# Kernel tuning notes

Measured on AMD Instinct MI355X. Metric: run time of the kernel, lower is better.

## Reference

```python
import jax, jax.numpy as jnp
import numpy as np

N = 10000       # nodes
E = 160000      # edges (avg degree 16)
F_IN = 5        # node feature dim
ED = 2          # edge feature dim


def _tconv(x, src, dst, ea, Wq, bq, Wk, bk, Wv, bv, We, Ws, bs, heads, C, concat):
    """PyG TransformerConv (eval mode, root_weight=True, beta=False)."""
    n = x.shape[0]
    q = (x @ Wq + bq).reshape(n, heads, C)
    k = (x @ Wk + bk).reshape(n, heads, C)
    v = (x @ Wv + bv).reshape(n, heads, C)
    e = (ea @ We).reshape(ea.shape[0], heads, C)          # edge embedding, added to key and value
    kj = k[src] + e                                        # [E,H,C] gather source keys
    vj = v[src] + e                                        # [E,H,C] gather source values
    logits = jnp.einsum('ehc,ehc->eh', q[dst], kj) / jnp.sqrt(jnp.asarray(C, x.dtype))
    m = jax.ops.segment_max(logits, dst, num_segments=n)   # stable segment softmax over in-edges
    p = jnp.exp(logits - m[dst])
    s = jax.ops.segment_sum(p, dst, num_segments=n)
    alpha = p / s[dst]                                     # [E,H]
    out = jax.ops.segment_sum(alpha[..., None] * vj, dst, num_segments=n)  # [N,H,C]
    out = out.reshape(n, heads * C) if concat else jnp.mean(out, axis=1)
    return out + x @ Ws + bs                               # root/skip connection


def setup_inputs() -> dict:
    key = jax.random.key(0)
    keys = iter(jax.random.split(key, 64))
    def p(shape):
        return jax.random.normal(next(keys), shape, jnp.float32) * 0.05
    inp = {}
    inp['x'] = jax.random.normal(next(keys), (N, F_IN), jnp.float32)
    inp['edge_src'] = jax.random.randint(next(keys), (E,), 0, N)
    inp['edge_dst'] = jax.random.randint(next(keys), (E,), 0, N)
    inp['edge_attr'] = jax.random.normal(next(keys), (E, ED), jnp.float32)
    # (in_dim, heads, out_channels, concat) for the 3 TransformerConv layers
    layers = [(F_IN, 4, 128, True), (512, 4, 128, True), (512, 1, 64, False)]
    for i, (fin, h, c, concat) in enumerate(layers, 1):
        hc = h * c
        sk = hc if concat else c
        inp[f'Wq{i}'] = p((fin, hc)); inp[f'bq{i}'] = p((hc,))
        inp[f'Wk{i}'] = p((fin, hc)); inp[f'bk{i}'] = p((hc,))
        inp[f'Wv{i}'] = p((fin, hc)); inp[f'bv{i}'] = p((hc,))
        inp[f'We{i}'] = p((ED, hc))   # lin_edge has no bias in PyG
        inp[f'Ws{i}'] = p((fin, sk)); inp[f'bs{i}'] = p((sk,))
    return inp


def reference(x, edge_src, edge_dst, edge_attr,
              Wq1, bq1, Wk1, bk1, Wv1, bv1, We1, Ws1, bs1,
              Wq2, bq2, Wk2, bk2, Wv2, bv2, We2, Ws2, bs2,
              Wq3, bq3, Wk3, bk3, Wv3, bv3, We3, Ws3, bs3):
    h = jax.nn.relu(_tconv(x, edge_src, edge_dst, edge_attr,
                           Wq1, bq1, Wk1, bk1, Wv1, bv1, We1, Ws1, bs1, 4, 128, True))
    h = jax.nn.relu(_tconv(h, edge_src, edge_dst, edge_attr,
                           Wq2, bq2, Wk2, bk2, Wv2, bv2, We2, Ws2, bs2, 4, 128, True))
    return _tconv(h, edge_src, edge_dst, edge_attr,
                  Wq3, bq3, Wk3, bk3, Wv3, bv3, We3, Ws3, bs3, 1, 64, False)
```

## Files before the change

kernel.cpp:

```cpp
#include <hip/hip_runtime.h>

typedef unsigned short u16;
typedef __attribute__((ext_vector_type(8))) short bf16x8;
typedef __attribute__((ext_vector_type(4))) float f32x4;

__device__ __forceinline__ float bf2f(u16 s) {
    return __uint_as_float(((unsigned)s) << 16);
}
__device__ __forceinline__ u16 f2bf(float f) {
    unsigned u = __float_as_uint(f);
    u += 0x7fff + ((u >> 16) & 1);
    return (u16)(u >> 16);
}
__device__ __forceinline__ void unpack8(bf16x8 x, float* f) {
#pragma unroll
    for (int j = 0; j < 8; ++j) f[j] = bf2f((u16)x[j]);
}

struct Ptr8 { const float* p[8]; };
struct PrepArgs { const float* w[8]; const float* b[8]; };

__global__ __launch_bounds__(256)
void prep_weights(PrepArgs a, u16* __restrict__ Wt2, u16* __restrict__ Wt3,
                  float* __restrict__ b2, float* __restrict__ b3) {
    int z = blockIdx.z;
    if (z == 8) {
        if (blockIdx.y != 0 || blockIdx.x >= 9) return;
        int j = blockIdx.x * 256 + threadIdx.x;
        if (j < 2048) b2[j] = a.b[j >> 9][j & 511];
        else if (j < 2304) { int jj = j - 2048; b3[jj] = a.b[4 + (jj >> 6)][jj & 63]; }
        return;
    }
    const float* in;
    u16* out;
    int Nw;
    if (z < 4) { in = a.w[z]; out = Wt2 + (size_t)z * 512 * 512; Nw = 512; }
    else {
        if (blockIdx.y >= 2) return;
        in = a.w[z]; out = Wt3 + (size_t)(z - 4) * 64 * 512; Nw = 64;
    }
    __shared__ float t[32][33];
    int kb = blockIdx.x * 32, nb = blockIdx.y * 32;
    int tx = threadIdx.x & 31, ty = threadIdx.x >> 5;
#pragma unroll
    for (int r = ty; r < 32; r += 8)
        if (nb + tx < Nw)
            t[r][tx] = in[(size_t)(kb + r) * Nw + nb + tx];
    __syncthreads();
#pragma unroll
    for (int r = ty; r < 32; r += 8)
        if (nb + r < Nw)
            out[(size_t)(nb + r) * 512 + kb + tx] = f2bf(t[tx][r]);
}

__global__ __launch_bounds__(256)
void gemm_l1(const float* __restrict__ X, Ptr8 wb, u16* __restrict__ OUT, int N) {
    int wsel = threadIdx.x >> 6;
    int jj = (threadIdx.x & 63) * 8;
    const float* W = wb.p[wsel];
    const float* b = wb.p[4 + wsel];
    float w[5][8], bs[8];
#pragma unroll
    for (int i = 0; i < 5; ++i)
#pragma unroll
        for (int j = 0; j < 8; ++j) w[i][j] = W[(size_t)i * 512 + jj + j];
#pragma unroll
    for (int j = 0; j < 8; ++j) bs[j] = b[jj + j];
    int n0 = blockIdx.x * 8;
    int nend = (N - n0 < 8) ? (N - n0) : 8;
    for (int i = 0; i < nend; ++i) {
        int n = n0 + i;
        float xr[5];
#pragma unroll
        for (int k = 0; k < 5; ++k) xr[k] = X[(size_t)n * 5 + k];
        float acc[8];
#pragma unroll
        for (int j = 0; j < 8; ++j) acc[j] = bs[j];
#pragma unroll
        for (int k = 0; k < 5; ++k)
#pragma unroll
            for (int j = 0; j < 8; ++j) acc[j] = fmaf(xr[k], w[k][j], acc[j]);
        bf16x8 o;
#pragma unroll
        for (int j = 0; j < 8; ++j) o[j] = (short)f2bf(acc[j]);
        *(bf16x8*)(OUT + (size_t)n * 2048 + wsel * 512 + jj) = o;
    }
}

template <int TN>
__global__ __launch_bounds__(256)
void gemm_bf16(const u16* __restrict__ A, const u16* __restrict__ Bt,
               const float* __restrict__ bias, u16* __restrict__ C,
               int M, int Ncols, int K) {
    constexpr int TM = 128, BK = 64;
    constexpr int MFR = (TN == 128) ? 4 : 2;
    constexpr int NFR = 4;
    constexpr int ACH = TM * BK / (256 * 8);
    constexpr int BCH = TN * BK / (256 * 8);

    __shared__ u16 As[TM * BK];
    __shared__ u16 Bs[TN * BK];

    int tid = threadIdx.x;
    int lane = tid & 63;
    int w = tid >> 6;
    int rowbase = blockIdx.x * TM;
    int colbase = blockIdx.y * TN;
    int mwave = (TN == 128) ? (w >> 1) * 64 : w * 32;
    int nwave = (TN == 128) ? (w & 1) * 64 : 0;

    f32x4 acc[MFR][NFR] = {};

    for (int k0 = 0; k0 < K; k0 += BK) {
        bf16x8 ra[ACH], rb[BCH];
#pragma unroll
        for (int c = 0; c < ACH; ++c) {
            int idx = c * 256 + tid;
            int row = idx >> 3, sl = idx & 7;
            int gr = rowbase + row; if (gr > M - 1) gr = M - 1;
            ra[c] = *(const bf16x8*)(A + (size_t)gr * K + k0 + sl * 8);
        }
#pragma unroll
        for (int c = 0; c < BCH; ++c) {
            int idx = c * 256 + tid;
            int row = idx >> 3, sl = idx & 7;
            rb[c] = *(const bf16x8*)(Bt + (size_t)(colbase + row) * K + k0 + sl * 8);
        }
        __syncthreads();
#pragma unroll
        for (int c = 0; c < ACH; ++c) {
            int idx = c * 256 + tid;
            int row = idx >> 3, sl = idx & 7;
            *(bf16x8*)&As[row * BK + ((sl ^ (row & 7)) * 8)] = ra[c];
        }
#pragma unroll
        for (int c = 0; c < BCH; ++c) {
            int idx = c * 256 + tid;
            int row = idx >> 3, sl = idx & 7;
            *(bf16x8*)&Bs[row * BK + ((sl ^ (row & 7)) * 8)] = rb[c];
        }
        __syncthreads();
#pragma unroll
        for (int kh = 0; kh < 2; ++kh) {
            bf16x8 af[MFR], bfr[NFR];
            int ks = (lane >> 4) + kh * 4;
#pragma unroll
            for (int mi = 0; mi < MFR; ++mi) {
                int r = mwave + mi * 16 + (lane & 15);
                af[mi] = *(const bf16x8*)&As[r * BK + ((ks ^ (r & 7)) * 8)];
            }
#pragma unroll
            for (int ni = 0; ni < NFR; ++ni) {
                int r = nwave + ni * 16 + (lane & 15);
                bfr[ni] = *(const bf16x8*)&Bs[r * BK + ((ks ^ (r & 7)) * 8)];
            }
#pragma unroll
            for (int mi = 0; mi < MFR; ++mi)
#pragma unroll
                for (int ni = 0; ni < NFR; ++ni)
                    acc[mi][ni] = __builtin_amdgcn_mfma_f32_16x16x32_bf16(
                        af[mi], bfr[ni], acc[mi][ni], 0, 0, 0);
        }
    }
#pragma unroll
    for (int mi = 0; mi < MFR; ++mi) {
        int r0 = rowbase + mwave + mi * 16 + (lane >> 4) * 4;
#pragma unroll
        for (int ni = 0; ni < NFR; ++ni) {
            int col = colbase + nwave + ni * 16 + (lane & 15);
            float bv = bias[col];
#pragma unroll
            for (int r = 0; r < 4; ++r) {
                int row = r0 + r;
                if (row < M)
                    C[(size_t)row * Ncols + col] = f2bf(acc[mi][ni][r] + bv);
            }
        }
    }
}

__global__ __launch_bounds__(256)
void histo_dst(const int* __restrict__ dst, int* __restrict__ deg, int E) {
    int i = blockIdx.x * 256 + threadIdx.x;
    if (i < E) atomicAdd(&deg[dst[i]], 1);
}

__global__ __launch_bounds__(1024)
void scan_deg(const int* __restrict__ deg, int* __restrict__ off,
              int* __restrict__ cur, int N) {
    __shared__ int part[1024];
    int t = threadIdx.x;
    int per = (N + 1023) / 1024;
    int base = t * per;
    int s = 0;
    for (int i = 0; i < per; ++i)
        if (base + i < N) s += deg[base + i];
    part[t] = s;
    __syncthreads();
    for (int d = 1; d < 1024; d <<= 1) {
        int v = (t >= d) ? part[t - d] : 0;
        __syncthreads();
        part[t] += v;
        __syncthreads();
    }
    int excl = (t > 0) ? part[t - 1] : 0;
    for (int i = 0; i < per; ++i) {
        int n = base + i;
        if (n < N) {
            off[n] = excl;
            cur[n] = excl;
            excl += deg[n];
        }
    }
    if (t == 1023) off[N] = part[1023];
}

__global__ __launch_bounds__(256)
void scatter_edges(const int* __restrict__ src, const int* __restrict__ dst,
                   const float* __restrict__ EA, int* __restrict__ cur,
                   int* __restrict__ csrc, float2* __restrict__ caxy, int E) {
    int i = blockIdx.x * 256 + threadIdx.x;
    if (i < E) {
        int p = atomicAdd(&cur[dst[i]], 1);
        csrc[p] = src[i];
        caxy[p] = *(const float2*)(EA + 2 * (size_t)i);
    }
}

template <int H, int C, int LPG, int EPAR, bool RELU, typename OutT>
__global__ __launch_bounds__(256)
void node_attn(const u16* __restrict__ QKVS, int SR, int koff, int voff,
               int skoff, const int* __restrict__ csrc,
               const float2* __restrict__ caxy, const float* __restrict__ We,
               const int* __restrict__ off, OutT* __restrict__ OUT,
               int OST, int N, float scale) {
    constexpr int HC = H * C;
    constexpr int NG = 64 / LPG;
    int n = blockIdx.x * 4 + (threadIdx.x >> 6);
    if (n >= N) return;
    int lane = threadIdx.x & 63;
    int g = lane / LPG;
    int li = lane % LPG;
    int cc = (EPAR > 1 ? 0 : g) * C + li * 8;

    const u16* nrow = QKVS + (size_t)n * SR;
    float q[8];
    unpack8(*(const bf16x8*)(nrow + cc), q);

    float qw0 = 0.f, qw1 = 0.f;
    {
        f32x4 wa = *(const f32x4*)(We + cc), wb = *(const f32x4*)(We + cc + 4);
        f32x4 wc = *(const f32x4*)(We + HC + cc), wd = *(const f32x4*)(We + HC + cc + 4);
#pragma unroll
        for (int j = 0; j < 4; ++j) {
            qw0 = fmaf(q[j], wa[j], qw0); qw0 = fmaf(q[4 + j], wb[j], qw0);
            qw1 = fmaf(q[j], wc[j], qw1); qw1 = fmaf(q[4 + j], wd[j], qw1);
        }
    }
#pragma unroll
    for (int d = 1; d < LPG; d <<= 1) {
        qw0 += __shfl_xor(qw0, d);
        qw1 += __shfl_xor(qw1, d);
    }

    int base = off[n];
    int deg = off[n + 1] - base;
    int pdeg = deg < 64 ? deg : 64;
    int ps = 0; float pax = 0.f, pay = 0.f;
    if (lane < pdeg) {
        ps = csrc[base + lane];
        float2 a = caxy[base + lane];
        pax = a.x; pay = a.y;
    }

    float m = -1e30f, s = 0.f, A0 = 0.f, A1 = 0.f;
    float acc[8] = {};
    const u16* Kp = QKVS + koff;
    const u16* Vp = QKVS + voff;

    auto process = [&](float ax, float ay, bf16x8 k8, bf16x8 v8) {
        float kf[8];
        unpack8(k8, kf);
        float qk = 0.f;
#pragma unroll
        for (int j = 0; j < 8; ++j) qk = fmaf(q[j], kf[j], qk);
#pragma unroll
        for (int d = 1; d < LPG; d <<= 1) qk += __shfl_xor(qk, d);
        float lg = scale * (qk + ax * qw0 + ay * qw1);
        if (lg > m + 8.f) {
            float r = __expf(m - lg);
            s *= r; A0 *= r; A1 *= r;
#pragma unroll
            for (int j = 0; j < 8; ++j) acc[j] *= r;
            m = lg;
        }
        float p = __expf(lg - m);
        s += p;
        A0 = fmaf(p, ax, A0);
        A1 = fmaf(p, ay, A1);
        float vf[8];
        unpack8(v8, vf);
#pragma unroll
        for (int j = 0; j < 8; ++j) acc[j] = fmaf(p, vf[j], acc[j]);
    };

    if constexpr (EPAR == 1) {
        auto ldp = [&](int t, bf16x8& k8, bf16x8& v8) {
            int tt = t < pdeg ? t : 0;
            int s0 = __shfl(ps, tt);
            k8 = *(const bf16x8*)(Kp + (size_t)s0 * SR + cc);
            v8 = *(const bf16x8*)(Vp + (size_t)s0 * SR + cc);
        };
        if (pdeg > 0) {
            bf16x8 ka0, va0, ka1, va1, kb0, vb0, kb1, vb1;
            ldp(0, ka0, va0); ldp(1, ka1, va1);
            ldp(2, kb0, vb0); ldp(3, kb1, vb1);
            int t = 0;
            for (; t + 2 < pdeg; t += 4) {
                float ax, ay;
                ax = __shfl(pax, t); ay = __shfl(pay, t);
                process(ax, ay, ka0, va0);
                ax = __shfl(pax, t + 1); ay = __shfl(pay, t + 1);
                process(ax, ay, ka1, va1);
                ldp(t + 4, ka0, va0); ldp(t + 5, ka1, va1);
                ax = __shfl(pax, t + 2); ay = __shfl(pay, t + 2);
                process(ax, ay, kb0, vb0);
                if (t + 3 < pdeg) {
                    ax = __shfl(pax, t + 3); ay = __shfl(pay, t + 3);
                    process(ax, ay, kb1, vb1);
                }
                ldp(t + 6, kb0, vb0); ldp(t + 7, kb1, vb1);
            }
            if (t < pdeg) {
                float ax = __shfl(pax, t), ay = __shfl(pay, t);
                process(ax, ay, ka0, va0);
            }
            if (t + 1 < pdeg) {
                float ax = __shfl(pax, t + 1), ay = __shfl(pay, t + 1);
                process(ax, ay, ka1, va1);
            }
        }
        for (int t = 64; t < deg; ++t) {
            int s0 = csrc[base + t];
            float2 a = caxy[base + t];
            bf16x8 k0 = *(const bf16x8*)(Kp + (size_t)s0 * SR + cc);
            bf16x8 v0 = *(const bf16x8*)(Vp + (size_t)s0 * SR + cc);
            process(a.x, a.y, k0, v0);
        }
    } else {
        int trips = (pdeg + NG - 1) / NG;
        for (int k = 0; k < trips; ++k) {
            int idx = g + NG * k;
            bool valid = idx < pdeg;
            int sidx = valid ? idx : (pdeg - 1);
            int s0 = __shfl(ps, sidx);
            float ax0 = __shfl(pax, sidx), ay0 = __shfl(pay, sidx);
            bf16x8 k0 = *(const bf16x8*)(Kp + (size_t)s0 * SR + cc);
            bf16x8 v0 = *(const bf16x8*)(Vp + (size_t)s0 * SR + cc);
            if (valid) process(ax0, ay0, k0, v0);
        }
        int otr = (deg > 64) ? (deg - 64 + NG - 1) / NG : 0;
        for (int k = 0; k < otr; ++k) {
            int idx = 64 + NG * k + g;
            bool valid = idx < deg;
            int ii = valid ? idx : (deg - 1);
            int s0 = csrc[base + ii];
            float2 a = caxy[base + ii];
            bf16x8 k0 = *(const bf16x8*)(Kp + (size_t)s0 * SR + cc);
            bf16x8 v0 = *(const bf16x8*)(Vp + (size_t)s0 * SR + cc);
            if (valid) process(a.x, a.y, k0, v0);
        }
#pragma unroll
        for (int d = LPG; d < 64; d <<= 1) {
            float mo = __shfl_xor(m, d), so = __shfl_xor(s, d);
            float A0o = __shfl_xor(A0, d), A1o = __shfl_xor(A1, d);
            float mn = fmaxf(m, mo);
            float ra = __expf(m - mn), rb = __expf(mo - mn);
            s = s * ra + so * rb;
            A0 = A0 * ra + A0o * rb;
            A1 = A1 * ra + A1o * rb;
#pragma unroll
            for (int j = 0; j < 8; ++j) {
                float ao = __shfl_xor(acc[j], d);
                acc[j] = acc[j] * ra + ao * rb;
            }
            m = mn;
        }
    }

    if (EPAR == 1 || g == 0) {
        float inv = (s > 0.f) ? 1.f / s : 0.f;
        float sk[8];
        unpack8(*(const bf16x8*)(nrow + skoff + cc), sk);
        f32x4 wa = *(const f32x4*)(We + cc), wb = *(const f32x4*)(We + cc + 4);
        f32x4 wc = *(const f32x4*)(We + HC + cc), wd = *(const f32x4*)(We + HC + cc + 4);
        float w0[8] = {wa[0], wa[1], wa[2], wa[3], wb[0], wb[1], wb[2], wb[3]};
        float w1[8] = {wc[0], wc[1], wc[2], wc[3], wd[0], wd[1], wd[2], wd[3]};
        float o[8];
#pragma unroll
        for (int j = 0; j < 8; ++j) {
            float agg = (acc[j] + A0 * w0[j] + A1 * w1[j]) * inv;
            o[j] = agg + sk[j];
            if (RELU) o[j] = fmaxf(o[j], 0.f);
        }
        if constexpr (sizeof(OutT) == 2) {
            bf16x8 ov;
#pragma unroll
            for (int j = 0; j < 8; ++j) ov[j] = (short)f2bf(o[j]);
            *(bf16x8*)((u16*)OUT + (size_t)n * OST + cc) = ov;
        } else {
            f32x4 oa = {o[0], o[1], o[2], o[3]}, ob = {o[4], o[5], o[6], o[7]};
            *(f32x4*)((float*)OUT + (size_t)n * OST + cc) = oa;
            *(f32x4*)((float*)OUT + (size_t)n * OST + cc + 4) = ob;
        }
    }
}

extern "C" void kernel_launch(void* const* d_in, const int* in_sizes, int n_in,
                              void* d_out, int out_size, void* d_ws, size_t ws_size,
                              hipStream_t stream) {
    const float* x  = (const float*)d_in[0];
    const int* esrc = (const int*)d_in[1];
    const int* edst = (const int*)d_in[2];
    const float* ea = (const float*)d_in[3];
    const int N = in_sizes[0] / 5;
    const int E = in_sizes[1];
    auto in = [&](int i) { return (const float*)d_in[i]; };

    char* p = (char*)d_ws;
    auto alloc = [&](size_t b) {
        char* r = p; p += (b + 255) & ~(size_t)255; return (void*)r;
    };
    u16* QKVS  = (u16*)alloc((size_t)N * 2048 * 2);
    u16* HB    = (u16*)alloc((size_t)N * 512 * 2);
    u16* Wt2   = (u16*)alloc((size_t)2048 * 512 * 2);
    u16* Wt3   = (u16*)alloc((size_t)256 * 512 * 2);
    float* b2  = (float*)alloc(2048 * 4);
    float* b3  = (float*)alloc(256 * 4);
    int* deg   = (int*)alloc((size_t)N * 4);
    int* off   = (int*)alloc((size_t)(N + 1) * 4);
    int* cur   = (int*)alloc((size_t)N * 4);
    int* csrc  = (int*)alloc((size_t)E * 4);
    float2* caxy = (float2*)alloc((size_t)E * 8);

    dim3 b256(256);
    int gE256 = (E + 255) / 256;
    int gM = (N + 127) / 128;
    int gA = (N + 3) / 4;
    const float scale128 = 0.08838834764831845f;
    const float scale64  = 0.125f;

    hipMemsetAsync(deg, 0, (size_t)N * sizeof(int), stream);
    histo_dst<<<gE256, b256, 0, stream>>>(edst, deg, E);
    scan_deg<<<1, 1024, 0, stream>>>(deg, off, cur, N);
    scatter_edges<<<gE256, b256, 0, stream>>>(esrc, edst, ea, cur, csrc, caxy, E);

    PrepArgs pa = {{in(13), in(15), in(17), in(20), in(22), in(24), in(26), in(29)},
                   {in(14), in(16), in(18), in(21), in(23), in(25), in(27), in(30)}};
    prep_weights<<<dim3(16, 16, 9), b256, 0, stream>>>(pa, Wt2, Wt3, b2, b3);

    Ptr8 l1 = {{in(4), in(6), in(8), in(11), in(5), in(7), in(9), in(12)}};
    gemm_l1<<<dim3((N + 7) / 8), b256, 0, stream>>>(x, l1, QKVS, N);
    node_attn<4, 128, 16, 1, true, u16><<<dim3(gA), b256, 0, stream>>>(
        QKVS, 2048, 512, 1024, 1536, csrc, caxy, in(10), off, HB, 512, N, scale128);

    gemm_bf16<128><<<dim3(gM, 16), b256, 0, stream>>>(HB, Wt2, b2, QKVS, N, 2048, 512);
    node_attn<4, 128, 16, 1, true, u16><<<dim3(gA), b256, 0, stream>>>(
        QKVS, 2048, 512, 1024, 1536, csrc, caxy, in(19), off, HB, 512, N, scale128);

    gemm_bf16<64><<<dim3(gM, 4), b256, 0, stream>>>(HB, Wt3, b3, QKVS, N, 256, 512);
    node_attn<1, 64, 8, 8, false, float><<<dim3(gA), b256, 0, stream>>>(
        QKVS, 256, 64, 128, 192, csrc, caxy, in(28), off,
        (float*)d_out, 64, N, scale64);
}
```

Before: 225.8 us.

## Split node edges across four waves per block for 4-head attention layers

Adds a node_attn4 kernel that gives each node a whole 256-thread block. The four waves each take every fourth in-edge, and the partial online-softmax states are merged through shared memory. The goal is to cut the serial per-node edge loop and raise memory-level parallelism for the gather-heavy layers 1 and 2. The cost is a __syncthreads, shared-memory traffic and a merge step, plus three of four waves sitting idle during the final write. The old generic kernel is reduced to the layer-3 path only.

```diff
diff --git a/kernel.cpp b/kernel.cpp
--- a/kernel.cpp
+++ b/kernel.cpp
@@ -227,6 +227,169 @@
     }
 }
 
+template <bool RELU>
+__global__ __launch_bounds__(256)
+void node_attn4(const u16* __restrict__ QKVS, const int* __restrict__ csrc,
+                const float2* __restrict__ caxy, const float* __restrict__ We,
+                const int* __restrict__ off, u16* __restrict__ OUT,
+                int N, float scale) {
+    constexpr int SR = 2048, koff = 512, voff = 1024, skoff = 1536;
+    constexpr int HC = 512, C = 128, LPG = 16;
+    int n = blockIdx.x;
+    int w = threadIdx.x >> 6;
+    int lane = threadIdx.x & 63;
+    int g = lane / LPG;
+    int li = lane % LPG;
+    int cc = g * C + li * 8;
+
+    const u16* nrow = QKVS + (size_t)n * SR;
+    float q[8];
+    unpack8(*(const bf16x8*)(nrow + cc), q);
+
+    float qw0 = 0.f, qw1 = 0.f;
+    {
+        f32x4 wa = *(const f32x4*)(We + cc), wb = *(const f32x4*)(We + cc + 4);
+        f32x4 wc = *(const f32x4*)(We + HC + cc), wd = *(const f32x4*)(We + HC + cc + 4);
+#pragma unroll
+        for (int j = 0; j < 4; ++j) {
+            qw0 = fmaf(q[j], wa[j], qw0); qw0 = fmaf(q[4 + j], wb[j], qw0);
+            qw1 = fmaf(q[j], wc[j], qw1); qw1 = fmaf(q[4 + j], wd[j], qw1);
+        }
+    }
+#pragma unroll
+    for (int d = 1; d < LPG; d <<= 1) {
+        qw0 += __shfl_xor(qw0, d);
+        qw1 += __shfl_xor(qw1, d);
+    }
+
+    int base = off[n];
+    int deg = off[n + 1] - base;
+    int pdeg = deg < 64 ? deg : 64;
+    int ps = 0; float pax = 0.f, pay = 0.f;
+    int el = w + 4 * lane;
+    if (lane < 16 && el < pdeg) {
+        ps = csrc[base + el];
+        float2 a = caxy[base + el];
+        pax = a.x; pay = a.y;
+    }
+    int wdeg = (pdeg > w) ? ((pdeg - w + 3) >> 2) : 0;
+
+    float m = -1e30f, s = 0.f, A0 = 0.f, A1 = 0.f;
+    float acc[8] = {};
+    const u16* Kp = QKVS + koff;
+    const u16* Vp = QKVS + voff;
+
+    auto process = [&](float ax, float ay, bf16x8 k8, bf16x8 v8) {
+        float kf[8];
+        unpack8(k8, kf);
+        float qk = 0.f;
+#pragma unroll
+        for (int j = 0; j < 8; ++j) qk = fmaf(q[j], kf[j], qk);
+#pragma unroll
+        for (int d = 1; d < LPG; d <<= 1) qk += __shfl_xor(qk, d);
+        float lg = scale * (qk + ax * qw0 + ay * qw1);
+        if (lg > m + 8.f) {
+            float r = __expf(m - lg);
+            s *= r; A0 *= r; A1 *= r;
+#pragma unroll
+            for (int j = 0; j < 8; ++j) acc[j] *= r;
+            m = lg;
+        }
+        float p = __expf(lg - m);
+        s += p;
+        A0 = fmaf(p, ax, A0);
+        A1 = fmaf(p, ay, A1);
+        float vf[8];
+        unpack8(v8, vf);
+#pragma unroll
+        for (int j = 0; j < 8; ++j) acc[j] = fmaf(p, vf[j], acc[j]);
+    };
+
+    auto ldp = [&](int t, bf16x8& k8, bf16x8& v8) {
+        int tt = t < wdeg ? t : 0;
+        int s0 = __shfl(ps, tt);
+        k8 = *(const bf16x8*)(Kp + (size_t)s0 * SR + cc);
+        v8 = *(const bf16x8*)(Vp + (size_t)s0 * SR + cc);
+    };
+    if (wdeg > 0) {
+        bf16x8 ka0, va0, ka1, va1, kb0, vb0, kb1, vb1;
+        ldp(0, ka0, va0); ldp(1, ka1, va1);
+        ldp(2, kb0, vb0); ldp(3, kb1, vb1);
+        int t = 0;
+        for (; t + 2 < wdeg; t += 4) {
+            float ax, ay;
+            ax = __shfl(pax, t); ay = __shfl(pay, t);
+            process(ax, ay, ka0, va0);
+            ax = __shfl(pax, t + 1); ay = __shfl(pay, t + 1);
+            process(ax, ay, ka1, va1);
+            ldp(t + 4, ka0, va0); ldp(t + 5, ka1, va1);
+            ax = __shfl(pax, t + 2); ay = __shfl(pay, t + 2);
+            process(ax, ay, kb0, vb0);
+            if (t + 3 < wdeg) {
+                ax = __shfl(pax, t + 3); ay = __shfl(pay, t + 3);
+                process(ax, ay, kb1, vb1);
+            }
+            ldp(t + 6, kb0, vb0); ldp(t + 7, kb1, vb1);
+        }
+        if (t < wdeg) {
+            float ax = __shfl(pax, t), ay = __shfl(pay, t);
+            process(ax, ay, ka0, va0);
+        }
+        if (t + 1 < wdeg) {
+            float ax = __shfl(pax, t + 1), ay = __shfl(pay, t + 1);
+            process(ax, ay, ka1, va1);
+        }
+    }
+    for (int idx = 64 + w; idx < deg; idx += 4) {
+        int s0 = csrc[base + idx];
+        float2 a = caxy[base + idx];
+        bf16x8 k0 = *(const bf16x8*)(Kp + (size_t)s0 * SR + cc);
+        bf16x8 v0 = *(const bf16x8*)(Vp + (size_t)s0 * SR + cc);
+        process(a.x, a.y, k0, v0);
+    }
+
+    __shared__ float sm[3][64][13];
+    if (w > 0) {
+        float* d = sm[w - 1][lane];
+        d[0] = m; d[1] = s; d[2] = A0; d[3] = A1;
+#pragma unroll
+        for (int j = 0; j < 8; ++j) d[4 + j] = acc[j];
+    }
+    __syncthreads();
+    if (w == 0) {
+#pragma unroll
+        for (int wv = 0; wv < 3; ++wv) {
+            const float* d = sm[wv][lane];
+            float mo = d[0], so = d[1], A0o = d[2], A1o = d[3];
+            float mn = fmaxf(m, mo);
+            float ra = __expf(m - mn), rb = __expf(mo - mn);
+            s = s * ra + so * rb;
+            A0 = A0 * ra + A0o * rb;
+            A1 = A1 * ra + A1o * rb;
+#pragma unroll
+            for (int j = 0; j < 8; ++j)
+                acc[j] = acc[j] * ra + d[4 + j] * rb;
+            m = mn;
+        }
+        float inv = (s > 0.f) ? 1.f / s : 0.f;
+        float sk[8];
+        unpack8(*(const bf16x8*)(nrow + skoff + cc), sk);
+        f32x4 wa = *(const f32x4*)(We + cc), wb = *(const f32x4*)(We + cc + 4);
+        f32x4 wc = *(const f32x4*)(We + HC + cc), wd = *(const f32x4*)(We + HC + cc + 4);
+        float w0[8] = {wa[0], wa[1], wa[2], wa[3], wb[0], wb[1], wb[2], wb[3]};
+        float w1[8] = {wc[0], wc[1], wc[2], wc[3], wd[0], wd[1], wd[2], wd[3]};
+        bf16x8 ov;
+#pragma unroll
+        for (int j = 0; j < 8; ++j) {
+            float agg = (acc[j] + A0 * w0[j] + A1 * w1[j]) * inv;
+            float o = agg + sk[j];
+            if (RELU) o = fmaxf(o, 0.f);
+            ov[j] = (short)f2bf(o);
+        }
+        *(bf16x8*)(OUT + (size_t)n * 512 + cc) = ov;
+    }
+}
+
 template <int H, int C, int LPG, int EPAR, bool RELU, typename OutT>
 __global__ __launch_bounds__(256)
 void node_attn(const u16* __restrict__ QKVS, int SR, int koff, int voff,
@@ -241,7 +404,7 @@
     int lane = threadIdx.x & 63;
     int g = lane / LPG;
     int li = lane % LPG;
-    int cc = (EPAR > 1 ? 0 : g) * C + li * 8;
+    int cc = li * 8;
 
     const u16* nrow = QKVS + (size_t)n * SR;
     float q[8];
@@ -304,91 +467,46 @@
         for (int j = 0; j < 8; ++j) acc[j] = fmaf(p, vf[j], acc[j]);
     };
 
-    if constexpr (EPAR == 1) {
-        auto ldp = [&](int t, bf16x8& k8, bf16x8& v8) {
-            int tt = t < pdeg ? t : 0;
-            int s0 = __shfl(ps, tt);
-            k8 = *(const bf16x8*)(Kp + (size_t)s0 * SR + cc);
-            v8 = *(const bf16x8*)(Vp + (size_t)s0 * SR + cc);
-        };
-        if (pdeg > 0) {
-            bf16x8 ka0, va0, ka1, va1, kb0, vb0, kb1, vb1;
-            ldp(0, ka0, va0); ldp(1, ka1, va1);
-            ldp(2, kb0, vb0); ldp(3, kb1, vb1);
-            int t = 0;
-            for (; t + 2 < pdeg; t += 4) {
-                float ax, ay;
-                ax = __shfl(pax, t); ay = __shfl(pay, t);
-                process(ax, ay, ka0, va0);
-                ax = __shfl(pax, t + 1); ay = __shfl(pay, t + 1);
-                process(ax, ay, ka1, va1);
-                ldp(t + 4, ka0, va0); ldp(t + 5, ka1, va1);
-                ax = __shfl(pax, t + 2); ay = __shfl(pay, t + 2);
-                process(ax, ay, kb0, vb0);
-                if (t + 3 < pdeg) {
-                    ax = __shfl(pax, t + 3); ay = __shfl(pay, t + 3);
-                    process(ax, ay, kb1, vb1);
-                }
-                ldp(t + 6, kb0, vb0); ldp(t + 7, kb1, vb1);
-            }
-            if (t < pdeg) {
-                float ax = __shfl(pax, t), ay = __shfl(pay, t);
-                process(ax, ay, ka0, va0);
-            }
-            if (t + 1 < pdeg) {
-                float ax = __shfl(pax, t + 1), ay = __shfl(pay, t + 1);
-                process(ax, ay, ka1, va1);
-            }
-        }
-        for (int t = 64; t < deg; ++t) {
-            int s0 = csrc[base + t];
-            float2 a = caxy[base + t];
-            bf16x8 k0 = *(const bf16x8*)(Kp + (size_t)s0 * SR + cc);
-            bf16x8 v0 = *(const bf16x8*)(Vp + (size_t)s0 * SR + cc);
-            process(a.x, a.y, k0, v0);
-        }
-    } else {
-        int trips = (pdeg + NG - 1) / NG;
-        for (int k = 0; k < trips; ++k) {
-            int idx = g + NG * k;
-            bool valid = idx < pdeg;
-            int sidx = valid ? idx : (pdeg - 1);
-            int s0 = __shfl(ps, sidx);
-            float ax0 = __shfl(pax, sidx), ay0 = __shfl(pay, sidx);
-            bf16x8 k0 = *(const bf16x8*)(Kp + (size_t)s0 * SR + cc);
-            bf16x8 v0 = *(const bf16x8*)(Vp + (size_t)s0 * SR + cc);
-            if (valid) process(ax0, ay0, k0, v0);
-        }
-        int otr = (deg > 64) ? (deg - 64 + NG - 1) / NG : 0;
-        for (int k = 0; k < otr; ++k) {
-            int idx = 64 + NG * k + g;
-            bool valid = idx < deg;
-            int ii = valid ? idx : (deg - 1);
-            int s0 = csrc[base + ii];
-            float2 a = caxy[base + ii];
-            bf16x8 k0 = *(const bf16x8*)(Kp + (size_t)s0 * SR + cc);
-            bf16x8 v0 = *(const bf16x8*)(Vp + (size_t)s0 * SR + cc);
-            if (valid) process(a.x, a.y, k0, v0);
-        }
-#pragma unroll
-        for (int d = LPG; d < 64; d <<= 1) {
-            float mo = __shfl_xor(m, d), so = __shfl_xor(s, d);
-            float A0o = __shfl_xor(A0, d), A1o = __shfl_xor(A1, d);
-            float mn = fmaxf(m, mo);
-            float ra = __expf(m - mn), rb = __expf(mo - mn);
-            s = s * ra + so * rb;
-            A0 = A0 * ra + A0o * rb;
-            A1 = A1 * ra + A1o * rb;
-#pragma unroll
-            for (int j = 0; j < 8; ++j) {
-                float ao = __shfl_xor(acc[j], d);
-                acc[j] = acc[j] * ra + ao * rb;
-            }
-            m = mn;
-        }
-    }
-
-    if (EPAR == 1 || g == 0) {
+    int trips = (pdeg + NG - 1) / NG;
+    for (int k = 0; k < trips; ++k) {
+        int idx = g + NG * k;
+        bool valid = idx < pdeg;
+        int sidx = valid ? idx : (pdeg - 1);
+        int s0 = __shfl(ps, sidx);
+        float ax0 = __shfl(pax, sidx), ay0 = __shfl(pay, sidx);
+        bf16x8 k0 = *(const bf16x8*)(Kp + (size_t)s0 * SR + cc);
+        bf16x8 v0 = *(const bf16x8*)(Vp + (size_t)s0 * SR + cc);
+        if (valid) process(ax0, ay0, k0, v0);
+    }
+    int otr = (deg > 64) ? (deg - 64 + NG - 1) / NG : 0;
+    for (int k = 0; k < otr; ++k) {
+        int idx = 64 + NG * k + g;
+        bool valid = idx < deg;
+        int ii = valid ? idx : (deg - 1);
+        int s0 = csrc[base + ii];
+        float2 a = caxy[base + ii];
+        bf16x8 k0 = *(const bf16x8*)(Kp + (size_t)s0 * SR + cc);
+        bf16x8 v0 = *(const bf16x8*)(Vp + (size_t)s0 * SR + cc);
+        if (valid) process(a.x, a.y, k0, v0);
+    }
+#pragma unroll
+    for (int d = LPG; d < 64; d <<= 1) {
+        float mo = __shfl_xor(m, d), so = __shfl_xor(s, d);
+        float A0o = __shfl_xor(A0, d), A1o = __shfl_xor(A1, d);
+        float mn = fmaxf(m, mo);
+        float ra = __expf(m - mn), rb = __expf(mo - mn);
+        s = s * ra + so * rb;
+        A0 = A0 * ra + A0o * rb;
+        A1 = A1 * ra + A1o * rb;
+#pragma unroll
+        for (int j = 0; j < 8; ++j) {
+            float ao = __shfl_xor(acc[j], d);
+            acc[j] = acc[j] * ra + ao * rb;
+        }
+        m = mn;
+    }
+
+    if (g == 0) {
         float inv = (s > 0.f) ? 1.f / s : 0.f;
         float sk[8];
         unpack8(*(const bf16x8*)(nrow + skoff + cc), sk);
@@ -403,16 +521,9 @@
             o[j] = agg + sk[j];
             if (RELU) o[j] = fmaxf(o[j], 0.f);
         }
-        if constexpr (sizeof(OutT) == 2) {
-            bf16x8 ov;
-#pragma unroll
-            for (int j = 0; j < 8; ++j) ov[j] = (short)f2bf(o[j]);
-            *(bf16x8*)((u16*)OUT + (size_t)n * OST + cc) = ov;
-        } else {
-            f32x4 oa = {o[0], o[1], o[2], o[3]}, ob = {o[4], o[5], o[6], o[7]};
-            *(f32x4*)((float*)OUT + (size_t)n * OST + cc) = oa;
-            *(f32x4*)((float*)OUT + (size_t)n * OST + cc + 4) = ob;
-        }
+        f32x4 oa = {o[0], o[1], o[2], o[3]}, ob = {o[4], o[5], o[6], o[7]};
+        *(f32x4*)((float*)OUT + (size_t)n * OST + cc) = oa;
+        *(f32x4*)((float*)OUT + (size_t)n * OST + cc + 4) = ob;
     }
 }
 
@@ -446,7 +557,6 @@
     dim3 b256(256);
     int gE256 = (E + 255) / 256;
     int gM = (N + 127) / 128;
-    int gA = (N + 3) / 4;
     const float scale128 = 0.08838834764831845f;
     const float scale64  = 0.125f;
 
@@ -461,15 +571,15 @@
 
     Ptr8 l1 = {{in(4), in(6), in(8), in(11), in(5), in(7), in(9), in(12)}};
     gemm_l1<<<dim3((N + 7) / 8), b256, 0, stream>>>(x, l1, QKVS, N);
-    node_attn<4, 128, 16, 1, true, u16><<<dim3(gA), b256, 0, stream>>>(
-        QKVS, 2048, 512, 1024, 1536, csrc, caxy, in(10), off, HB, 512, N, scale128);
+    node_attn4<true><<<dim3(N), b256, 0, stream>>>(
+        QKVS, csrc, caxy, in(10), off, HB, N, scale128);
 
     gemm_bf16<128><<<dim3(gM, 16), b256, 0, stream>>>(HB, Wt2, b2, QKVS, N, 2048, 512);
-    node_attn<4, 128, 16, 1, true, u16><<<dim3(gA), b256, 0, stream>>>(
-        QKVS, 2048, 512, 1024, 1536, csrc, caxy, in(19), off, HB, 512, N, scale128);
+    node_attn4<true><<<dim3(N), b256, 0, stream>>>(
+        QKVS, csrc, caxy, in(19), off, HB, N, scale128);
 
     gemm_bf16<64><<<dim3(gM, 4), b256, 0, stream>>>(HB, Wt3, b3, QKVS, N, 256, 512);
-    node_attn<1, 64, 8, 8, false, float><<<dim3(gA), b256, 0, stream>>>(
+    node_attn<1, 64, 8, 8, false, float><<<dim3((N + 3) / 4), b256, 0, stream>>>(
         QKVS, 256, 64, 128, 192, csrc, caxy, in(28), off,
         (float*)d_out, 64, N, scale64);
 }
```

New measurement: 224.1 us. About the same (-0.8%).
